# Kernel tuning notes

Hardware: AMD Instinct MI355X
Metric: run time of the kernel (lower is better)

## Reference

```python
import jax, jax.numpy as jnp
import numpy as np

LN_EPS = 1e-5

def _quantize(w):
    # round(W / mean|W|), clamp to {-1,0,1}, with straight-through estimator
    wq = jnp.clip(jnp.round(w / jnp.mean(jnp.abs(w))), -1.0, 1.0)
    return w + jax.lax.stop_gradient(wq - w)

def _ternary_linear(x, W, gamma, beta):
    mu = jnp.mean(x, axis=-1, keepdims=True)
    var = jnp.mean(jnp.square(x - mu), axis=-1, keepdims=True)
    xn = (x - mu) * jax.lax.rsqrt(var + LN_EPS) * gamma + beta
    return xn @ _quantize(W)

def setup_inputs() -> dict:
    key = jax.random.key(0)
    ks = jax.random.split(key, 10)
    B, T, E, H = 4, 4096, 1024, 64
    x = jax.random.normal(ks[0], (B, T, E), dtype=jnp.float32)
    Wk = jax.random.normal(ks[1], (E, H), dtype=jnp.float32)
    Wq = jax.random.normal(ks[2], (E, H), dtype=jnp.float32)
    Wv = jax.random.normal(ks[3], (E, H), dtype=jnp.float32)
    gk = jnp.ones((E,), jnp.float32); bk = jnp.zeros((E,), jnp.float32)
    gq = jnp.ones((E,), jnp.float32); bq = jnp.zeros((E,), jnp.float32)
    gv = jnp.ones((E,), jnp.float32); bv = jnp.zeros((E,), jnp.float32)
    return {"x": x, "Wk": Wk, "Wq": Wq, "Wv": Wv,
            "gk": gk, "bk": bk, "gq": gq, "bq": bq, "gv": gv, "bv": bv}

def reference(x, Wk, Wq, Wv, gk, bk, gq, bq, gv, bv):
    k = _ternary_linear(x, Wk, gk, bk)   # [B,T,H]
    q = _ternary_linear(x, Wq, gq, bq)   # [B,T,H]
    v = _ternary_linear(x, Wv, gv, bv)   # [B,T,H]
    scale = k.shape[-1] ** -0.5
    wei = jnp.einsum('bth,bsh->bts', q, k) * scale  # [B,T,T]
    wei = jax.nn.softmax(wei, axis=-1)              # dropout p=0 -> identity
    return jnp.einsum('bts,bsh->bth', wei, v)       # [B,T,H]
```

## Files before the change

kernel.cpp:

```cpp
#include <hip/hip_runtime.h>
#include <math.h>

#define LN_EPS 1e-5f

typedef __attribute__((ext_vector_type(8))) short    bf16x8;
typedef __attribute__((ext_vector_type(8))) _Float16 f16x8;
typedef __attribute__((ext_vector_type(4))) float    f32x4;

__device__ inline ushort f2bf(float f){
    union { float f; uint u; } v; v.f = f;
    uint r = v.u + 0x7fffu + ((v.u >> 16) & 1u);
    return (ushort)(r >> 16);
}
__device__ inline float bf2f(ushort h){
    union { uint u; float f; } v; v.u = ((uint)h) << 16;
    return v.f;
}
__device__ inline ushort f2h(float f){
    union { _Float16 h; ushort u; } v; v.h = (_Float16)f;
    return v.u;
}


__global__ __launch_bounds__(1024) void quant_k(
    const float* __restrict__ Wq, const float* __restrict__ Wk, const float* __restrict__ Wv,
    const float* __restrict__ gq, const float* __restrict__ bq,
    const float* __restrict__ gk, const float* __restrict__ bk,
    const float* __restrict__ gv, const float* __restrict__ bv,
    ushort* __restrict__ Wg_hi, ushort* __restrict__ Wg_lo,
    float* __restrict__ colsumg, float* __restrict__ cvec)
{
    const int br = blockIdx.x;
    const float* W = (br==0) ? Wq : (br==1 ? Wk : Wv);
    const float* g = (br==0) ? gq : (br==1 ? gk : gv);
    const float* bb= (br==0) ? bq : (br==1 ? bk : bv);
    const int t = threadIdx.x;
    __shared__ float red[1024];
    float s = 0.f;
    #pragma unroll 4
    for (int i=0;i<64;i++) s += fabsf(W[t + 1024*i]);
    red[t] = s;
    __syncthreads();
    for (int o=512;o>0;o>>=1){ if (t<o) red[t]+=red[t+o]; __syncthreads(); }
    const float mean = red[0] * (1.0f/65536.0f);

    const float ge = g[t];
    for (int h=0; h<64; h++) {
        float w  = W[t*64+h];
        float wq = fminf(1.f, fmaxf(-1.f, rintf(w/mean)));
        float wg = ge*wq;
        ushort hh = f2bf(wg);
        Wg_hi[(size_t)(br*64+h)*1024 + t] = hh;
        Wg_lo[(size_t)(br*64+h)*1024 + t] = f2bf(wg - bf2f(hh));
    }
    const int h2 = t & 63, chunk = t >> 6;
    float cg = 0.f, cb = 0.f;
    for (int i=0;i<64;i++){
        int e = chunk*64 + i;
        float w  = W[e*64+h2];
        float wq = fminf(1.f, fmaxf(-1.f, rintf(w/mean)));
        cg += g[e]*wq;
        cb += bb[e]*wq;
    }
    __shared__ float credg[16][64];
    __shared__ float credb[16][64];
    credg[chunk][h2] = cg;
    credb[chunk][h2] = cb;
    __syncthreads();
    if (t < 64){
        float sg = 0.f, sb = 0.f;
        #pragma unroll
        for (int i=0;i<16;i++){ sg += credg[i][t]; sb += credb[i][t]; }
        colsumg[br*64 + t] = sg;
        cvec[br*64 + t]    = sb;
    }
}

__global__ __launch_bounds__(256) void lngemm_k(
    const float* __restrict__ x, const ushort* __restrict__ Wg_hi,
    const ushort* __restrict__ Wg_lo, const float* __restrict__ colsumg,
    const float* __restrict__ cvec, float* __restrict__ qf,
    ushort* __restrict__ khi, ushort* __restrict__ klo,
    ushort* __restrict__ vthi, ushort* __restrict__ vtlo)
{
    __shared__ char smem[65536];
    __shared__ float mu_s[64], rs_s[64];
    char* Ah = smem;
    char* Al = smem + 8192;
    char* Bh = smem + 16384;
    char* Bl = smem + 40960;

    const int t  = threadIdx.x;
    const int r0 = blockIdx.x * 64;
    const int lane = t & 63, w = t >> 6, lr = lane & 15, lq = lane >> 4;
    const int arow = t >> 2, apart = t & 3;

    float4 ax[4];
    {
        const float* xp = x + (size_t)(r0+arow)*1024 + apart*16;
        ax[0]=*(const float4*)(xp);   ax[1]=*(const float4*)(xp+4);
        ax[2]=*(const float4*)(xp+8); ax[3]=*(const float4*)(xp+12);
    }
    uint4 bhv[3][2], blv[3][2];
    #pragma unroll
    for (int cc=0;cc<3;cc++){
        int id = cc*256 + t; int brow = id>>2; int bpart = id&3;
        const ushort* ph = Wg_hi + (size_t)brow*1024 + bpart*16;
        const ushort* pl = Wg_lo + (size_t)brow*1024 + bpart*16;
        bhv[cc][0]=*(const uint4*)(ph); bhv[cc][1]=*(const uint4*)(ph+8);
        blv[cc][0]=*(const uint4*)(pl); blv[cc][1]=*(const uint4*)(pl+8);
    }

    {
        const float* xr = x + (size_t)(r0 + arow)*1024 + apart*4;
        float s1=0.f, s2=0.f;
        #pragma unroll 8
        for (int j=0;j<64;j++){
            float4 v = *(const float4*)(xr + j*16);
            s1 += v.x+v.y+v.z+v.w;
            s2 += v.x*v.x+v.y*v.y+v.z*v.z+v.w*v.w;
        }
        s1 += __shfl_xor(s1,1); s1 += __shfl_xor(s1,2);
        s2 += __shfl_xor(s2,1); s2 += __shfl_xor(s2,2);
        if (apart==0){
            float mu  = s1*(1.f/1024.f);
            float var = s2*(1.f/1024.f) - mu*mu;
            mu_s[arow]=mu; rs_s[arow]=rsqrtf(var+LN_EPS);
        }
    }

    f32x4 acc[12];
    #pragma unroll
    for (int n=0;n<12;n++) acc[n] = (f32x4){0.f,0.f,0.f,0.f};

    const int aswz = (arow&7)<<4;

    for (int kt=0; kt<16; kt++){
        {
            float xs[16] = {ax[0].x,ax[0].y,ax[0].z,ax[0].w,
                            ax[1].x,ax[1].y,ax[1].z,ax[1].w,
                            ax[2].x,ax[2].y,ax[2].z,ax[2].w,
                            ax[3].x,ax[3].y,ax[3].z,ax[3].w};
            uint hu[8], lu[8];
            #pragma unroll
            for (int j=0;j<8;j++){
                ushort h0 = f2bf(xs[2*j]),   h1 = f2bf(xs[2*j+1]);
                ushort l0 = f2bf(xs[2*j]  - bf2f(h0));
                ushort l1 = f2bf(xs[2*j+1]- bf2f(h1));
                hu[j] = (uint)h0 | ((uint)h1<<16);
                lu[j] = (uint)l0 | ((uint)l1<<16);
            }
            *(uint4*)(Ah + arow*128 + ((apart*32)    ^ aswz)) = (uint4){hu[0],hu[1],hu[2],hu[3]};
            *(uint4*)(Ah + arow*128 + ((apart*32+16) ^ aswz)) = (uint4){hu[4],hu[5],hu[6],hu[7]};
            *(uint4*)(Al + arow*128 + ((apart*32)    ^ aswz)) = (uint4){lu[0],lu[1],lu[2],lu[3]};
            *(uint4*)(Al + arow*128 + ((apart*32+16) ^ aswz)) = (uint4){lu[4],lu[5],lu[6],lu[7]};
            #pragma unroll
            for (int cc=0;cc<3;cc++){
                int id = cc*256 + t; int brow = id>>2; int bpart = id&3;
                int bswz = (brow&7)<<4;
                *(uint4*)(Bh + brow*128 + ((bpart*32)    ^ bswz)) = bhv[cc][0];
                *(uint4*)(Bh + brow*128 + ((bpart*32+16) ^ bswz)) = bhv[cc][1];
                *(uint4*)(Bl + brow*128 + ((bpart*32)    ^ bswz)) = blv[cc][0];
                *(uint4*)(Bl + brow*128 + ((bpart*32+16) ^ bswz)) = blv[cc][1];
            }
        }
        __syncthreads();
        if (kt < 15){
            const float* xp = x + (size_t)(r0+arow)*1024 + (kt+1)*64 + apart*16;
            ax[0]=*(const float4*)(xp);   ax[1]=*(const float4*)(xp+4);
            ax[2]=*(const float4*)(xp+8); ax[3]=*(const float4*)(xp+12);
            #pragma unroll
            for (int cc=0;cc<3;cc++){
                int id = cc*256 + t; int brow = id>>2; int bpart = id&3;
                const ushort* ph = Wg_hi + (size_t)brow*1024 + (kt+1)*64 + bpart*16;
                const ushort* pl = Wg_lo + (size_t)brow*1024 + (kt+1)*64 + bpart*16;
                bhv[cc][0]=*(const uint4*)(ph); bhv[cc][1]=*(const uint4*)(ph+8);
                blv[cc][0]=*(const uint4*)(pl); blv[cc][1]=*(const uint4*)(pl+8);
            }
        }
        #pragma unroll
        for (int kc=0;kc<2;kc++){
            const int abc = kc*64 + lq*16;
            const int ar  = w*16 + lr;
            const int aoff = ar*128 + (abc ^ ((ar&7)<<4));
            bf16x8 ah = *(const bf16x8*)(Ah + aoff);
            bf16x8 al = *(const bf16x8*)(Al + aoff);
            #pragma unroll
            for (int n=0;n<12;n++){
                const int br2 = n*16 + lr;
                const int boff = br2*128 + (abc ^ ((br2&7)<<4));
                bf16x8 bh = *(const bf16x8*)(Bh + boff);
                bf16x8 bl = *(const bf16x8*)(Bl + boff);
                acc[n] = __builtin_amdgcn_mfma_f32_16x16x32_bf16(ah, bh, acc[n], 0,0,0);
                acc[n] = __builtin_amdgcn_mfma_f32_16x16x32_bf16(al, bh, acc[n], 0,0,0);
                acc[n] = __builtin_amdgcn_mfma_f32_16x16x32_bf16(ah, bl, acc[n], 0,0,0);
            }
        }
        __syncthreads();
    }

    #pragma unroll
    for (int n=0;n<12;n++){
        const int col = n*16 + lr;
        const float csg = colsumg[col];
        const float cv  = cvec[col];
        #pragma unroll
        for (int i=0;i<4;i++){
            const int lrow = w*16 + lq*4 + i;
            const int grow = r0 + lrow;
            float val = rs_s[lrow]*(acc[n][i] - mu_s[lrow]*csg) + cv;
            if (col < 64){
                qf[(size_t)grow*64 + col] = val;
            } else if (col < 128){
                ushort hh = f2bf(val);
                khi[(size_t)grow*64 + (col-64)] = hh;
                klo[(size_t)grow*64 + (col-64)] = f2h(val - bf2f(hh));
            } else {
                const int b2 = grow >> 12, tt = grow & 4095, hcol = col - 128;
                ushort hh = f2bf(val);
                vthi[((size_t)b2*64 + hcol)*4096 + tt] = hh;
                vtlo[((size_t)b2*64 + hcol)*4096 + tt] = f2bf(val - bf2f(hh));
            }
        }
    }
}

__global__ __launch_bounds__(256, 2) void attn_mfma_k(
    const float* __restrict__ qf, const ushort* __restrict__ khi,
    const ushort* __restrict__ klo, const ushort* __restrict__ vthi,
    const ushort* __restrict__ vtlo, float* __restrict__ Opart,
    float* __restrict__ ml, int tps)
{
    __shared__ char smem[32768];

    const int t    = threadIdx.x;
    const int lane = t & 63;
    const int w    = t >> 6;
    const int lr   = lane & 15;
    const int lq   = lane >> 4;

    const int bid = blockIdx.x, nwg = gridDim.x;
    const int virt = (bid & 7) * (nwg >> 3) + (bid >> 3);
    const int ks = virt >> 8;
    const int b  = (virt >> 6) & 3;
    const int qt = virt & 63;

    const int gq = b*4096 + qt*64 + w*16 + lr;
    bf16x8 aqh[2]; f16x8 aqh16[2], aql16[2];
    #pragma unroll
    for (int ks2=0; ks2<2; ks2++){
        const float* qp = qf + (size_t)gq*64 + ks2*32 + lq*8;
        float4 qa = *(const float4*)(qp);
        float4 qb = *(const float4*)(qp+4);
        float qv[8] = {qa.x,qa.y,qa.z,qa.w,qb.x,qb.y,qb.z,qb.w};
        #pragma unroll
        for (int j=0;j<8;j++){
            float q = qv[j] * 0.125f;
            ushort hb = f2bf(q);
            float  hf = bf2f(hb);
            aqh[ks2][j]   = (short)hb;
            aqh16[ks2][j] = (_Float16)hf;
            aql16[ks2][j] = (_Float16)(q - hf);
        }
    }

    float m_[4], l_[4];
    f32x4 Oacc[4];
    #pragma unroll
    for (int i=0;i<4;i++){ m_[i] = -3.0e38f; l_[i] = 0.f; }
    #pragma unroll
    for (int n=0;n<4;n++) Oacc[n] = (f32x4){0.f,0.f,0.f,0.f};

    const int srow = t >> 2;
    const int sseg = (t & 3) * 32;
    const int sd0 = srow*128 + (sseg ^ ((srow&7)<<4));
    const int sd1 = srow*128 + ((sseg+16) ^ ((srow&7)<<4));

    for (int kt = ks*tps; kt < ks*tps + tps; kt++){
        __syncthreads();
        {
            const int grow = b*4096 + kt*64 + srow;
            const char* skh = (const char*)(khi + (size_t)grow*64) + sseg;
            const char* skl = (const char*)(klo + (size_t)grow*64) + sseg;
            const char* svh = (const char*)(vthi + ((size_t)b*64 + srow)*4096 + kt*64) + sseg;
            const char* svl = (const char*)(vtlo + ((size_t)b*64 + srow)*4096 + kt*64) + sseg;
            *(uint4*)(smem         + sd0) = *(const uint4*)(skh);
            *(uint4*)(smem         + sd1) = *(const uint4*)(skh+16);
            *(uint4*)(smem +  8192 + sd0) = *(const uint4*)(skl);
            *(uint4*)(smem +  8192 + sd1) = *(const uint4*)(skl+16);
            *(uint4*)(smem + 16384 + sd0) = *(const uint4*)(svh);
            *(uint4*)(smem + 16384 + sd1) = *(const uint4*)(svh+16);
            *(uint4*)(smem + 24576 + sd0) = *(const uint4*)(svl);
            *(uint4*)(smem + 24576 + sd1) = *(const uint4*)(svl+16);
        }
        __syncthreads();

        f32x4 sacc[4];
        #pragma unroll
        for (int n=0;n<4;n++) sacc[n] = (f32x4){0.f,0.f,0.f,0.f};
        #pragma unroll
        for (int ks2=0; ks2<2; ks2++){
            #pragma unroll
            for (int n=0;n<4;n++){
                const int row = n*16 + lr;
                const int bc  = (ks2*32 + lq*8)*2;
                const int off = row*128 + (bc ^ ((row&7)<<4));
                bf16x8 bkh = *(const bf16x8*)(smem + off);
                f16x8  bkl = *(const f16x8*)(smem + 8192 + off);
                f16x8  bkh16;
                #pragma unroll
                for (int j=0;j<8;j++) bkh16[j] = (_Float16)bf2f((ushort)bkh[j]);
                sacc[n] = __builtin_amdgcn_mfma_f32_16x16x32_bf16(aqh[ks2],  bkh,   sacc[n], 0,0,0);
                sacc[n] = __builtin_amdgcn_mfma_f32_16x16x32_f16 (aqh16[ks2], bkl,  sacc[n], 0,0,0);
                sacc[n] = __builtin_amdgcn_mfma_f32_16x16x32_f16 (aql16[ks2], bkh16,sacc[n], 0,0,0);
                sacc[n] = __builtin_amdgcn_mfma_f32_16x16x32_f16 (aql16[ks2], bkl,  sacc[n], 0,0,0);
            }
        }

        float pvals[4][4];
        float al[4];
        #pragma unroll
        for (int i=0;i<4;i++){
            float tm = fmaxf(fmaxf(sacc[0][i],sacc[1][i]), fmaxf(sacc[2][i],sacc[3][i]));
            tm = fmaxf(tm, __shfl_xor(tm,1));
            tm = fmaxf(tm, __shfl_xor(tm,2));
            tm = fmaxf(tm, __shfl_xor(tm,4));
            tm = fmaxf(tm, __shfl_xor(tm,8));
            float mn = fmaxf(m_[i], tm);
            float a  = __expf(m_[i] - mn);
            float rs = 0.f;
            #pragma unroll
            for (int n=0;n<4;n++){
                float p = __expf(sacc[n][i] - mn);
                pvals[n][i] = p;
                rs += p;
            }
            rs += __shfl_xor(rs,1);
            rs += __shfl_xor(rs,2);
            rs += __shfl_xor(rs,4);
            rs += __shfl_xor(rs,8);
            l_[i] = l_[i]*a + rs;
            m_[i] = mn;
            al[i] = a;
        }
        #pragma unroll
        for (int n=0;n<4;n++){
            #pragma unroll
            for (int i=0;i<4;i++) Oacc[n][i] *= al[i];
        }

        __syncthreads();
        char* Pw = smem + w*4096;
        #pragma unroll
        for (int n=0;n<4;n++){
            #pragma unroll
            for (int i=0;i<4;i++){
                const int row = lq*4 + i;
                const int bc  = (n*16 + lr)*4;
                float  p  = pvals[n][i];
                ushort ph = f2bf(p);
                ushort pl = f2bf(p - bf2f(ph));
                *(uint*)(Pw + row*256 + (bc ^ ((row&7)<<4))) = (uint)ph | ((uint)pl << 16);
            }
        }
        asm volatile("s_waitcnt lgkmcnt(0)" ::: "memory");

        #pragma unroll
        for (int ks2=0; ks2<2; ks2++){
            const int pbc = ks2*128 + lq*32;
            uint4 pv0 = *(const uint4*)(Pw + lr*256 + ( pbc      ^ ((lr&7)<<4)));
            uint4 pv1 = *(const uint4*)(Pw + lr*256 + ((pbc+16)  ^ ((lr&7)<<4)));
            uint pu[8] = {pv0.x,pv0.y,pv0.z,pv0.w,pv1.x,pv1.y,pv1.z,pv1.w};
            bf16x8 ph, pl;
            #pragma unroll
            for (int j=0;j<8;j++){
                ph[j] = (short)(pu[j] & 0xffffu);
                pl[j] = (short)(pu[j] >> 16);
            }
            #pragma unroll
            for (int n=0;n<4;n++){
                const int row = n*16 + lr;
                const int bc  = (ks2*32 + lq*8)*2;
                const int off = row*128 + (bc ^ ((row&7)<<4));
                bf16x8 bvh = *(const bf16x8*)(smem + 16384 + off);
                bf16x8 bvl = *(const bf16x8*)(smem + 24576 + off);
                Oacc[n] = __builtin_amdgcn_mfma_f32_16x16x32_bf16(ph, bvh, Oacc[n], 0,0,0);
                Oacc[n] = __builtin_amdgcn_mfma_f32_16x16x32_bf16(ph, bvl, Oacc[n], 0,0,0);
                Oacc[n] = __builtin_amdgcn_mfma_f32_16x16x32_bf16(pl, bvh, Oacc[n], 0,0,0);
            }
        }
    }

    #pragma unroll
    for (int n=0;n<4;n++){
        #pragma unroll
        for (int i=0;i<4;i++){
            const int row = b*4096 + qt*64 + w*16 + lq*4 + i;
            Opart[((size_t)ks*16384 + row)*64 + n*16 + lr] = Oacc[n][i];
        }
    }
    if (lr == 0){
        #pragma unroll
        for (int i=0;i<4;i++){
            const int row = b*4096 + qt*64 + w*16 + lq*4 + i;
            ml[((size_t)ks*16384 + row)*2 + 0] = m_[i];
            ml[((size_t)ks*16384 + row)*2 + 1] = l_[i];
        }
    }
}

__global__ __launch_bounds__(256) void combine_k(
    const float* __restrict__ Opart, const float* __restrict__ ml,
    float* __restrict__ out, int nsplit)
{
    const int t = threadIdx.x;
    const int tx = t & 15, ty = t >> 4;
    const int r = blockIdx.x * 16 + ty;
    float mstar = -3.0e38f;
    for (int s=0;s<nsplit;s++)
        mstar = fmaxf(mstar, ml[((size_t)s*16384 + r)*2]);
    float lstar = 0.f;
    float4 o = make_float4(0.f,0.f,0.f,0.f);
    for (int s=0;s<nsplit;s++){
        float ms = ml[((size_t)s*16384 + r)*2];
        float ls = ml[((size_t)s*16384 + r)*2 + 1];
        float wgt = __expf(ms - mstar);
        lstar += wgt * ls;
        float4 p = *(const float4*)(Opart + ((size_t)s*16384 + r)*64 + tx*4);
        o.x += wgt*p.x; o.y += wgt*p.y; o.z += wgt*p.z; o.w += wgt*p.w;
    }
    float inv = 1.0f / lstar;
    o.x*=inv; o.y*=inv; o.z*=inv; o.w*=inv;
    *(float4*)(out + (size_t)r*64 + tx*4) = o;
}

extern "C" void kernel_launch(void* const* d_in, const int* in_sizes, int n_in,
                              void* d_out, int out_size, void* d_ws, size_t ws_size,
                              hipStream_t stream) {
    const float* x  = (const float*)d_in[0];
    const float* Wk = (const float*)d_in[1];
    const float* Wq = (const float*)d_in[2];
    const float* Wv = (const float*)d_in[3];
    const float* gk = (const float*)d_in[4];
    const float* bk = (const float*)d_in[5];
    const float* gq = (const float*)d_in[6];
    const float* bq = (const float*)d_in[7];
    const float* gv = (const float*)d_in[8];
    const float* bv = (const float*)d_in[9];
    float* out = (float*)d_out;
    char* ws = (char*)d_ws;
    ushort* Wg_hi   = (ushort*)(ws);
    ushort* Wg_lo   = (ushort*)(ws + 393216);
    float*  colsumg = (float*)(ws + 786432);
    float*  cvec    = (float*)(ws + 787200);
    float*  qf   = (float*)(ws + 1048576);
    ushort* khi  = (ushort*)(ws + 5242880);
    ushort* klo  = (ushort*)(ws + 7340032);
    ushort* vthi = (ushort*)(ws + 9437184);
    ushort* vtlo = (ushort*)(ws + 11534336);

    const size_t base = 13631488;
    int ns;
    if      (ws_size >= base + 4ull*4325376) ns = 4;
    else if (ws_size >= base + 2ull*4325376) ns = 2;
    else                                     ns = 1;
    float* Opart = (float*)(ws + base);
    float* mlp   = (float*)(ws + base + (size_t)ns*4194304);

    quant_k<<<dim3(3), dim3(1024), 0, stream>>>(Wq, Wk, Wv, gq, bq, gk, bk, gv, bv,
                                                Wg_hi, Wg_lo, colsumg, cvec);
    lngemm_k<<<dim3(256), dim3(256), 0, stream>>>(x, Wg_hi, Wg_lo, colsumg, cvec,
                                                  qf, khi, klo, vthi, vtlo);
    attn_mfma_k<<<dim3(256*ns), dim3(256), 0, stream>>>(qf, khi, klo, vthi, vtlo, Opart, mlp, 64/ns);
    combine_k<<<dim3(1024), dim3(256), 0, stream>>>(Opart, mlp, out, ns);
}
```

Measured before the change: 326.0 us.

## Switch split-precision MFMA from bf16 to fp16 and skip zero low-weight terms

Replaces the bf16 hi/lo splits with fp16 hi/lo splits in the LN-GEMM and attention kernels. This drops the fourth QK MFMA and the per-element bf16-to-fp16 conversion of K, and lets P be stored as separate fp16 planes. The quantize kernel now sets a flag when the fp16 low part of gamma*Wq is nonzero, and the GEMM skips loading and multiplying the low weight plane when it is zero. The risk is fp16 range overflow for large activations, and the flag check adds a branch to the GEMM.

```diff
diff --git a/kernel.cpp b/kernel.cpp
--- a/kernel.cpp
+++ b/kernel.cpp
@@ -3,22 +3,16 @@
 
 #define LN_EPS 1e-5f
 
-typedef __attribute__((ext_vector_type(8))) short    bf16x8;
 typedef __attribute__((ext_vector_type(8))) _Float16 f16x8;
 typedef __attribute__((ext_vector_type(4))) float    f32x4;
 
-__device__ inline ushort f2bf(float f){
-    union { float f; uint u; } v; v.f = f;
-    uint r = v.u + 0x7fffu + ((v.u >> 16) & 1u);
-    return (ushort)(r >> 16);
-}
-__device__ inline float bf2f(ushort h){
-    union { uint u; float f; } v; v.u = ((uint)h) << 16;
-    return v.f;
-}
 __device__ inline ushort f2h(float f){
     union { _Float16 h; ushort u; } v; v.h = (_Float16)f;
     return v.u;
+}
+__device__ inline float h2f(ushort u){
+    union { ushort u; _Float16 h; } v; v.u = u;
+    return (float)v.h;
 }
 
 
@@ -27,8 +21,8 @@
     const float* __restrict__ gq, const float* __restrict__ bq,
     const float* __restrict__ gk, const float* __restrict__ bk,
     const float* __restrict__ gv, const float* __restrict__ bv,
-    ushort* __restrict__ Wg_hi, ushort* __restrict__ Wg_lo,
-    float* __restrict__ colsumg, float* __restrict__ cvec)
+    ushort* __restrict__ Wh16, ushort* __restrict__ Wl16,
+    float* __restrict__ colsumg, float* __restrict__ cvec, int* __restrict__ flags)
 {
     const int br = blockIdx.x;
     const float* W = (br==0) ? Wq : (br==1 ? Wk : Wv);
@@ -36,23 +30,29 @@
     const float* bb= (br==0) ? bq : (br==1 ? bk : bv);
     const int t = threadIdx.x;
     __shared__ float red[1024];
+    __shared__ int nzs;
     float s = 0.f;
     #pragma unroll 4
     for (int i=0;i<64;i++) s += fabsf(W[t + 1024*i]);
     red[t] = s;
+    if (t==0) nzs = 0;
     __syncthreads();
     for (int o=512;o>0;o>>=1){ if (t<o) red[t]+=red[t+o]; __syncthreads(); }
     const float mean = red[0] * (1.0f/65536.0f);
 
     const float ge = g[t];
+    int nz = 0;
     for (int h=0; h<64; h++) {
         float w  = W[t*64+h];
         float wq = fminf(1.f, fmaxf(-1.f, rintf(w/mean)));
         float wg = ge*wq;
-        ushort hh = f2bf(wg);
-        Wg_hi[(size_t)(br*64+h)*1024 + t] = hh;
-        Wg_lo[(size_t)(br*64+h)*1024 + t] = f2bf(wg - bf2f(hh));
-    }
+        ushort hh = f2h(wg);
+        ushort ll = f2h(wg - h2f(hh));
+        Wh16[(size_t)(br*64+h)*1024 + t] = hh;
+        Wl16[(size_t)(br*64+h)*1024 + t] = ll;
+        nz |= (int)(ll & 0x7fffu);
+    }
+    if (nz) atomicOr(&nzs, 1);
     const int h2 = t & 63, chunk = t >> 6;
     float cg = 0.f, cb = 0.f;
     for (int i=0;i<64;i++){
@@ -74,14 +74,16 @@
         colsumg[br*64 + t] = sg;
         cvec[br*64 + t]    = sb;
     }
+    if (t == 0) flags[br] = nzs;
 }
 
 __global__ __launch_bounds__(256) void lngemm_k(
-    const float* __restrict__ x, const ushort* __restrict__ Wg_hi,
-    const ushort* __restrict__ Wg_lo, const float* __restrict__ colsumg,
-    const float* __restrict__ cvec, float* __restrict__ qf,
-    ushort* __restrict__ khi, ushort* __restrict__ klo,
-    ushort* __restrict__ vthi, ushort* __restrict__ vtlo)
+    const float* __restrict__ x, const ushort* __restrict__ Wh16,
+    const ushort* __restrict__ Wl16, const float* __restrict__ colsumg,
+    const float* __restrict__ cvec, const int* __restrict__ flags,
+    float* __restrict__ qf,
+    ushort* __restrict__ kh16, ushort* __restrict__ kl16,
+    ushort* __restrict__ vth, ushort* __restrict__ vtl)
 {
     __shared__ char smem[65536];
     __shared__ float mu_s[64], rs_s[64];
@@ -94,6 +96,7 @@
     const int r0 = blockIdx.x * 64;
     const int lane = t & 63, w = t >> 6, lr = lane & 15, lq = lane >> 4;
     const int arow = t >> 2, apart = t & 3;
+    const int flag = flags[0] | flags[1] | flags[2];
 
     float4 ax[4];
     {
@@ -105,10 +108,12 @@
     #pragma unroll
     for (int cc=0;cc<3;cc++){
         int id = cc*256 + t; int brow = id>>2; int bpart = id&3;
-        const ushort* ph = Wg_hi + (size_t)brow*1024 + bpart*16;
-        const ushort* pl = Wg_lo + (size_t)brow*1024 + bpart*16;
+        const ushort* ph = Wh16 + (size_t)brow*1024 + bpart*16;
         bhv[cc][0]=*(const uint4*)(ph); bhv[cc][1]=*(const uint4*)(ph+8);
-        blv[cc][0]=*(const uint4*)(pl); blv[cc][1]=*(const uint4*)(pl+8);
+        if (flag){
+            const ushort* pl = Wl16 + (size_t)brow*1024 + bpart*16;
+            blv[cc][0]=*(const uint4*)(pl); blv[cc][1]=*(const uint4*)(pl+8);
+        }
     }
 
     {
@@ -144,9 +149,9 @@
             uint hu[8], lu[8];
             #pragma unroll
             for (int j=0;j<8;j++){
-                ushort h0 = f2bf(xs[2*j]),   h1 = f2bf(xs[2*j+1]);
-                ushort l0 = f2bf(xs[2*j]  - bf2f(h0));
-                ushort l1 = f2bf(xs[2*j+1]- bf2f(h1));
+                ushort h0 = f2h(xs[2*j]),    h1 = f2h(xs[2*j+1]);
+                ushort l0 = f2h(xs[2*j]   - h2f(h0));
+                ushort l1 = f2h(xs[2*j+1] - h2f(h1));
                 hu[j] = (uint)h0 | ((uint)h1<<16);
                 lu[j] = (uint)l0 | ((uint)l1<<16);
             }
@@ -160,8 +165,10 @@
                 int bswz = (brow&7)<<4;
                 *(uint4*)(Bh + brow*128 + ((bpart*32)    ^ bswz)) = bhv[cc][0];
                 *(uint4*)(Bh + brow*128 + ((bpart*32+16) ^ bswz)) = bhv[cc][1];
-                *(uint4*)(Bl + brow*128 + ((bpart*32)    ^ bswz)) = blv[cc][0];
-                *(uint4*)(Bl + brow*128 + ((bpart*32+16) ^ bswz)) = blv[cc][1];
+                if (flag){
+                    *(uint4*)(Bl + brow*128 + ((bpart*32)    ^ bswz)) = blv[cc][0];
+                    *(uint4*)(Bl + brow*128 + ((bpart*32+16) ^ bswz)) = blv[cc][1];
+                }
             }
         }
         __syncthreads();
@@ -172,10 +179,12 @@
             #pragma unroll
             for (int cc=0;cc<3;cc++){
                 int id = cc*256 + t; int brow = id>>2; int bpart = id&3;
-                const ushort* ph = Wg_hi + (size_t)brow*1024 + (kt+1)*64 + bpart*16;
-                const ushort* pl = Wg_lo + (size_t)brow*1024 + (kt+1)*64 + bpart*16;
+                const ushort* ph = Wh16 + (size_t)brow*1024 + (kt+1)*64 + bpart*16;
                 bhv[cc][0]=*(const uint4*)(ph); bhv[cc][1]=*(const uint4*)(ph+8);
-                blv[cc][0]=*(const uint4*)(pl); blv[cc][1]=*(const uint4*)(pl+8);
+                if (flag){
+                    const ushort* pl = Wl16 + (size_t)brow*1024 + (kt+1)*64 + bpart*16;
+                    blv[cc][0]=*(const uint4*)(pl); blv[cc][1]=*(const uint4*)(pl+8);
+                }
             }
         }
         #pragma unroll
@@ -183,17 +192,19 @@
             const int abc = kc*64 + lq*16;
             const int ar  = w*16 + lr;
             const int aoff = ar*128 + (abc ^ ((ar&7)<<4));
-            bf16x8 ah = *(const bf16x8*)(Ah + aoff);
-            bf16x8 al = *(const bf16x8*)(Al + aoff);
+            f16x8 ah = *(const f16x8*)(Ah + aoff);
+            f16x8 al = *(const f16x8*)(Al + aoff);
             #pragma unroll
             for (int n=0;n<12;n++){
                 const int br2 = n*16 + lr;
                 const int boff = br2*128 + (abc ^ ((br2&7)<<4));
-                bf16x8 bh = *(const bf16x8*)(Bh + boff);
-                bf16x8 bl = *(const bf16x8*)(Bl + boff);
-                acc[n] = __builtin_amdgcn_mfma_f32_16x16x32_bf16(ah, bh, acc[n], 0,0,0);
-                acc[n] = __builtin_amdgcn_mfma_f32_16x16x32_bf16(al, bh, acc[n], 0,0,0);
-                acc[n] = __builtin_amdgcn_mfma_f32_16x16x32_bf16(ah, bl, acc[n], 0,0,0);
+                f16x8 bh = *(const f16x8*)(Bh + boff);
+                acc[n] = __builtin_amdgcn_mfma_f32_16x16x32_f16(ah, bh, acc[n], 0,0,0);
+                acc[n] = __builtin_amdgcn_mfma_f32_16x16x32_f16(al, bh, acc[n], 0,0,0);
+                if (flag){
+                    f16x8 bl = *(const f16x8*)(Bl + boff);
+                    acc[n] = __builtin_amdgcn_mfma_f32_16x16x32_f16(ah, bl, acc[n], 0,0,0);
+                }
             }
         }
         __syncthreads();
@@ -212,23 +223,23 @@
             if (col < 64){
                 qf[(size_t)grow*64 + col] = val;
             } else if (col < 128){
-                ushort hh = f2bf(val);
-                khi[(size_t)grow*64 + (col-64)] = hh;
-                klo[(size_t)grow*64 + (col-64)] = f2h(val - bf2f(hh));
+                ushort hh = f2h(val);
+                kh16[(size_t)grow*64 + (col-64)] = hh;
+                kl16[(size_t)grow*64 + (col-64)] = f2h(val - h2f(hh));
             } else {
                 const int b2 = grow >> 12, tt = grow & 4095, hcol = col - 128;
-                ushort hh = f2bf(val);
-                vthi[((size_t)b2*64 + hcol)*4096 + tt] = hh;
-                vtlo[((size_t)b2*64 + hcol)*4096 + tt] = f2bf(val - bf2f(hh));
+                ushort hh = f2h(val);
+                vth[((size_t)b2*64 + hcol)*4096 + tt] = hh;
+                vtl[((size_t)b2*64 + hcol)*4096 + tt] = f2h(val - h2f(hh));
             }
         }
     }
 }
 
 __global__ __launch_bounds__(256, 2) void attn_mfma_k(
-    const float* __restrict__ qf, const ushort* __restrict__ khi,
-    const ushort* __restrict__ klo, const ushort* __restrict__ vthi,
-    const ushort* __restrict__ vtlo, float* __restrict__ Opart,
+    const float* __restrict__ qf, const ushort* __restrict__ kh16,
+    const ushort* __restrict__ kl16, const ushort* __restrict__ vth,
+    const ushort* __restrict__ vtl, float* __restrict__ Opart,
     float* __restrict__ ml, int tps)
 {
     __shared__ char smem[32768];
@@ -246,7 +257,7 @@
     const int qt = virt & 63;
 
     const int gq = b*4096 + qt*64 + w*16 + lr;
-    bf16x8 aqh[2]; f16x8 aqh16[2], aql16[2];
+    f16x8 aqh[2], aql[2];
     #pragma unroll
     for (int ks2=0; ks2<2; ks2++){
         const float* qp = qf + (size_t)gq*64 + ks2*32 + lq*8;
@@ -256,11 +267,9 @@
         #pragma unroll
         for (int j=0;j<8;j++){
             float q = qv[j] * 0.125f;
-            ushort hb = f2bf(q);
-            float  hf = bf2f(hb);
-            aqh[ks2][j]   = (short)hb;
-            aqh16[ks2][j] = (_Float16)hf;
-            aql16[ks2][j] = (_Float16)(q - hf);
+            _Float16 qh = (_Float16)q;
+            aqh[ks2][j] = qh;
+            aql[ks2][j] = (_Float16)(q - (float)qh);
         }
     }
 
@@ -280,10 +289,10 @@
         __syncthreads();
         {
             const int grow = b*4096 + kt*64 + srow;
-            const char* skh = (const char*)(khi + (size_t)grow*64) + sseg;
-            const char* skl = (const char*)(klo + (size_t)grow*64) + sseg;
-            const char* svh = (const char*)(vthi + ((size_t)b*64 + srow)*4096 + kt*64) + sseg;
-            const char* svl = (const char*)(vtlo + ((size_t)b*64 + srow)*4096 + kt*64) + sseg;
+            const char* skh = (const char*)(kh16 + (size_t)grow*64) + sseg;
+            const char* skl = (const char*)(kl16 + (size_t)grow*64) + sseg;
+            const char* svh = (const char*)(vth + ((size_t)b*64 + srow)*4096 + kt*64) + sseg;
+            const char* svl = (const char*)(vtl + ((size_t)b*64 + srow)*4096 + kt*64) + sseg;
             *(uint4*)(smem         + sd0) = *(const uint4*)(skh);
             *(uint4*)(smem         + sd1) = *(const uint4*)(skh+16);
             *(uint4*)(smem +  8192 + sd0) = *(const uint4*)(skl);
@@ -305,15 +314,11 @@
                 const int row = n*16 + lr;
                 const int bc  = (ks2*32 + lq*8)*2;
                 const int off = row*128 + (bc ^ ((row&7)<<4));
-                bf16x8 bkh = *(const bf16x8*)(smem + off);
-                f16x8  bkl = *(const f16x8*)(smem + 8192 + off);
-                f16x8  bkh16;
-                #pragma unroll
-                for (int j=0;j<8;j++) bkh16[j] = (_Float16)bf2f((ushort)bkh[j]);
-                sacc[n] = __builtin_amdgcn_mfma_f32_16x16x32_bf16(aqh[ks2],  bkh,   sacc[n], 0,0,0);
-                sacc[n] = __builtin_amdgcn_mfma_f32_16x16x32_f16 (aqh16[ks2], bkl,  sacc[n], 0,0,0);
-                sacc[n] = __builtin_amdgcn_mfma_f32_16x16x32_f16 (aql16[ks2], bkh16,sacc[n], 0,0,0);
-                sacc[n] = __builtin_amdgcn_mfma_f32_16x16x32_f16 (aql16[ks2], bkl,  sacc[n], 0,0,0);
+                f16x8 bkh = *(const f16x8*)(smem + off);
+                f16x8 bkl = *(const f16x8*)(smem + 8192 + off);
+                sacc[n] = __builtin_amdgcn_mfma_f32_16x16x32_f16(aqh[ks2], bkh, sacc[n], 0,0,0);
+                sacc[n] = __builtin_amdgcn_mfma_f32_16x16x32_f16(aql[ks2], bkh, sacc[n], 0,0,0);
+                sacc[n] = __builtin_amdgcn_mfma_f32_16x16x32_f16(aqh[ks2], bkl, sacc[n], 0,0,0);
             }
         }
 
@@ -350,43 +355,39 @@
         }
 
         __syncthreads();
-        char* Pw = smem + w*4096;
+        char* Ph = smem + w*4096;
+        char* Pl = Ph + 2048;
         #pragma unroll
         for (int n=0;n<4;n++){
             #pragma unroll
             for (int i=0;i<4;i++){
                 const int row = lq*4 + i;
-                const int bc  = (n*16 + lr)*4;
-                float  p  = pvals[n][i];
-                ushort ph = f2bf(p);
-                ushort pl = f2bf(p - bf2f(ph));
-                *(uint*)(Pw + row*256 + (bc ^ ((row&7)<<4))) = (uint)ph | ((uint)pl << 16);
+                const int bc  = (n*16 + lr)*2;
+                const int ad  = row*128 + (bc ^ ((row&7)<<4));
+                float  p   = pvals[n][i];
+                ushort ph_ = f2h(p);
+                *(ushort*)(Ph + ad) = ph_;
+                *(ushort*)(Pl + ad) = f2h(p - h2f(ph_));
             }
         }
         asm volatile("s_waitcnt lgkmcnt(0)" ::: "memory");
 
         #pragma unroll
         for (int ks2=0; ks2<2; ks2++){
-            const int pbc = ks2*128 + lq*32;
-            uint4 pv0 = *(const uint4*)(Pw + lr*256 + ( pbc      ^ ((lr&7)<<4)));
-            uint4 pv1 = *(const uint4*)(Pw + lr*256 + ((pbc+16)  ^ ((lr&7)<<4)));
-            uint pu[8] = {pv0.x,pv0.y,pv0.z,pv0.w,pv1.x,pv1.y,pv1.z,pv1.w};
-            bf16x8 ph, pl;
-            #pragma unroll
-            for (int j=0;j<8;j++){
-                ph[j] = (short)(pu[j] & 0xffffu);
-                pl[j] = (short)(pu[j] >> 16);
-            }
+            const int pbyte = ks2*64 + lq*16;
+            const int poff  = lr*128 + (pbyte ^ ((lr&7)<<4));
+            f16x8 ph = *(const f16x8*)(Ph + poff);
+            f16x8 pl = *(const f16x8*)(Pl + poff);
             #pragma unroll
             for (int n=0;n<4;n++){
                 const int row = n*16 + lr;
                 const int bc  = (ks2*32 + lq*8)*2;
                 const int off = row*128 + (bc ^ ((row&7)<<4));
-                bf16x8 bvh = *(const bf16x8*)(smem + 16384 + off);
-                bf16x8 bvl = *(const bf16x8*)(smem + 24576 + off);
-                Oacc[n] = __builtin_amdgcn_mfma_f32_16x16x32_bf16(ph, bvh, Oacc[n], 0,0,0);
-                Oacc[n] = __builtin_amdgcn_mfma_f32_16x16x32_bf16(ph, bvl, Oacc[n], 0,0,0);
-                Oacc[n] = __builtin_amdgcn_mfma_f32_16x16x32_bf16(pl, bvh, Oacc[n], 0,0,0);
+                f16x8 bvh = *(const f16x8*)(smem + 16384 + off);
+                f16x8 bvl = *(const f16x8*)(smem + 24576 + off);
+                Oacc[n] = __builtin_amdgcn_mfma_f32_16x16x32_f16(ph, bvh, Oacc[n], 0,0,0);
+                Oacc[n] = __builtin_amdgcn_mfma_f32_16x16x32_f16(ph, bvl, Oacc[n], 0,0,0);
+                Oacc[n] = __builtin_amdgcn_mfma_f32_16x16x32_f16(pl, bvh, Oacc[n], 0,0,0);
             }
         }
     }
@@ -449,15 +450,16 @@
     const float* bv = (const float*)d_in[9];
     float* out = (float*)d_out;
     char* ws = (char*)d_ws;
-    ushort* Wg_hi   = (ushort*)(ws);
-    ushort* Wg_lo   = (ushort*)(ws + 393216);
+    ushort* Wh16    = (ushort*)(ws);
+    ushort* Wl16    = (ushort*)(ws + 393216);
     float*  colsumg = (float*)(ws + 786432);
     float*  cvec    = (float*)(ws + 787200);
+    int*    flags   = (int*)(ws + 787968);
     float*  qf   = (float*)(ws + 1048576);
-    ushort* khi  = (ushort*)(ws + 5242880);
-    ushort* klo  = (ushort*)(ws + 7340032);
-    ushort* vthi = (ushort*)(ws + 9437184);
-    ushort* vtlo = (ushort*)(ws + 11534336);
+    ushort* kh16 = (ushort*)(ws + 5242880);
+    ushort* kl16 = (ushort*)(ws + 7340032);
+    ushort* vth  = (ushort*)(ws + 9437184);
+    ushort* vtl  = (ushort*)(ws + 11534336);
 
     const size_t base = 13631488;
     int ns;
@@ -468,9 +470,9 @@
     float* mlp   = (float*)(ws + base + (size_t)ns*4194304);
 
     quant_k<<<dim3(3), dim3(1024), 0, stream>>>(Wq, Wk, Wv, gq, bq, gk, bk, gv, bv,
-                                                Wg_hi, Wg_lo, colsumg, cvec);
-    lngemm_k<<<dim3(256), dim3(256), 0, stream>>>(x, Wg_hi, Wg_lo, colsumg, cvec,
-                                                  qf, khi, klo, vthi, vtlo);
-    attn_mfma_k<<<dim3(256*ns), dim3(256), 0, stream>>>(qf, khi, klo, vthi, vtlo, Opart, mlp, 64/ns);
+                                                Wh16, Wl16, colsumg, cvec, flags);
+    lngemm_k<<<dim3(256), dim3(256), 0, stream>>>(x, Wh16, Wl16, colsumg, cvec, flags,
+                                                  qf, kh16, kl16, vth, vtl);
+    attn_mfma_k<<<dim3(256*ns), dim3(256), 0, stream>>>(qf, kh16, kl16, vth, vtl, Opart, mlp, 64/ns);
     combine_k<<<dim3(1024), dim3(256), 0, stream>>>(Opart, mlp, out, ns);
 }
```

Result: faster. 293.9 us (-9.8%).
